# Performance work log

Measured on AMD Instinct MI355X. Metric: run time of the kernel, lower is better.

## Reference

```python
import jax, jax.numpy as jnp
import numpy as np

D, FIN1, CL1_F, CL1_K, CL2_F, CL2_K, FC1_F, FC2_F = 4096, 1, 32, 25, 64, 25, 512, 10
B = 64
NNZ1, NNZ2 = D * 8, (D // 2) * 8
LMAX = 2.0  # lmax_L of a normalized graph Laplacian
FC1FIN = CL2_F * (D // 4)


def setup_inputs() -> dict:
    key = jax.random.key(0)
    ks = jax.random.split(key, 16)
    def lin(kw, fout, fin):
        scale = np.sqrt(2.0 / (fin + fout)).astype(np.float32)
        return jax.random.uniform(kw, (fout, fin), jnp.float32, -scale, scale)
    V2 = D // 2
    return {
        "x": jax.random.normal(ks[0], (B, D, FIN1), jnp.float32),
        "L1_rows": jax.random.randint(ks[1], (NNZ1,), 0, D),
        "L1_cols": jax.random.randint(ks[2], (NNZ1,), 0, D),
        "L1_vals": jax.random.normal(ks[3], (NNZ1,), jnp.float32) * 0.1,
        "L2_rows": jax.random.randint(ks[4], (NNZ2,), 0, V2),
        "L2_cols": jax.random.randint(ks[5], (NNZ2,), 0, V2),
        "L2_vals": jax.random.normal(ks[6], (NNZ2,), jnp.float32) * 0.1,
        "cl1_W": lin(ks[7], CL1_F, CL1_K * FIN1),
        "cl1_b": jnp.zeros((CL1_F,), jnp.float32),
        "cl2_W": lin(ks[8], CL2_F, CL2_K * CL1_F),
        "cl2_b": jnp.zeros((CL2_F,), jnp.float32),
        "fc1_W": lin(ks[9], FC1_F, FC1FIN),
        "fc1_b": jnp.zeros((FC1_F,), jnp.float32),
        "fc2_W": lin(ks[10], FC2_F, FC1_F),
        "fc2_b": jnp.zeros((FC2_F,), jnp.float32),
    }


def _cheby_conv(x, rows, cols, vals, W, b, K):
    # x: [B, V, Fin]; sparse rescaled Laplacian Ls = (2/lmax)*L - I applied as SpMM.
    Bn, V, Fin = x.shape
    x0 = jnp.transpose(x, (1, 2, 0)).reshape(V, Fin * Bn)  # [V, Fin*B]
    coef = jnp.asarray(2.0 / LMAX, x.dtype)

    def Ls(z):  # (2/lmax) * L @ z - z, via segment-sum SpMM
        return coef * jax.ops.segment_sum(vals[:, None] * z[cols], rows, num_segments=V) - z

    xs = [x0]
    if K > 1:
        x1 = Ls(x0)
        xs.append(x1)
    for _ in range(2, K):
        x2 = 2.0 * Ls(x1) - x0
        xs.append(x2)
        x0, x1 = x1, x2
    xk = jnp.stack(xs, 0).reshape(K, V, Fin, Bn)        # [K, V, Fin, B]
    xk = jnp.transpose(xk, (3, 1, 2, 0)).reshape(Bn * V, Fin * K)
    y = xk @ W.T + b
    return y.reshape(Bn, V, -1)


def _max_pool(x, p):
    # max-pool over node dim with stride p (matches MaxPool1d over permuted layout)
    Bn, V, F = x.shape
    return x.reshape(Bn, V // p, p, F).max(axis=2)


def reference(x, L1_rows, L1_cols, L1_vals, L2_rows, L2_cols, L2_vals,
              cl1_W, cl1_b, cl2_W, cl2_b, fc1_W, fc1_b, fc2_W, fc2_b):
    h = _cheby_conv(x, L1_rows, L1_cols, L1_vals, cl1_W, cl1_b, CL1_K)
    h = jax.nn.relu(h)
    h = _max_pool(h, 2)
    h = _cheby_conv(h, L2_rows, L2_cols, L2_vals, cl2_W, cl2_b, CL2_K)
    h = jax.nn.relu(h)
    h = _max_pool(h, 2)
    h = h.reshape(-1, FC1FIN)
    h = jax.nn.relu(h @ fc1_W.T + fc1_b)
    # dropout d=0.0 (eval/deterministic) -> identity
    return h @ fc2_W.T + fc2_b
```

## Files before the change

kernel.cpp:

```cpp
#include <hip/hip_runtime.h>
#include <hip/hip_bf16.h>

#define V1 4096
#define V2 2048
#define NNZ1 32768
#define NNZ2 16384
#define WCAP 48

typedef unsigned short u16;
typedef unsigned int u32;
typedef __attribute__((ext_vector_type(8))) short bf16x8;
typedef __attribute__((ext_vector_type(4))) float f32x4;

static __device__ __forceinline__ float bf2f(u16 u) {
  union { u32 i; float f; } c; c.i = ((u32)u) << 16; return c.f;
}
static __device__ __forceinline__ u16 f2bf(float f) {
  union { u32 i; float f; } c; c.f = f;
  u32 r = c.i + 0x7FFFu + ((c.i >> 16) & 1u);
  return (u16)(r >> 16);
}

__global__ void k_hist(const int* __restrict__ L1r, const int* __restrict__ L2r,
                       const float* __restrict__ W2, u16* __restrict__ Wh,
                       u16* __restrict__ Wl,
                       int* __restrict__ cnt1, int* __restrict__ cnt2) {
  int lt = blockIdx.x, t = threadIdx.x;
  if (lt < 128) {
    atomicAdd(&cnt1[L1r[lt * 256 + t]], 1);
  } else if (lt < 192) {
    atomicAdd(&cnt2[L2r[(lt - 128) * 256 + t]], 1);
  } else {
    int idx = (lt - 192) * 256 + t;
    int f = idx / 800;
    int kap = idx - f * 800;
    int k = kap >> 5, fin = kap & 31;
    float w = W2[f * 800 + fin * 25 + k];
    u16 hi = f2bf(w);
    Wh[idx] = hi;
    Wl[idx] = f2bf(w - bf2f(hi));
  }
}

__global__ void k_scan(int* __restrict__ cnt1, int* __restrict__ rs1,
                       int* __restrict__ cnt2, int* __restrict__ rs2,
                       int* __restrict__ slotOf1, int* __restrict__ rowOf1,
                       int* __restrict__ slotOf2, int* __restrict__ rowOf2) {
  __shared__ int sums[256];
  __shared__ int degS[V1];
  __shared__ int hist[64];
  __shared__ int hb[64];
  int t = threadIdx.x;
  int* cnt; int* rs; int* slotOf; int* rowOf; int V, NT, nnz;
  if (blockIdx.x == 0) { cnt = cnt1; rs = rs1; slotOf = slotOf1; rowOf = rowOf1; V = V1; NT = 1024; nnz = NNZ1; }
  else                 { cnt = cnt2; rs = rs2; slotOf = slotOf2; rowOf = rowOf2; V = V2; NT = 512;  nnz = NNZ2; }
  int chunk = V / 256, base = t * chunk, s = 0;
  for (int i = 0; i < chunk; ++i) { int c = cnt[base + i]; degS[base + i] = c; s += c; }
  sums[t] = s;
  if (t < 64) hist[t] = 0;
  __syncthreads();
  if (t == 0) {
    int run = 0;
    for (int i = 0; i < 256; ++i) { int c = sums[i]; sums[i] = run; run += c; }
  }
  __syncthreads();
  int pfx = sums[t];
  for (int i = 0; i < chunk; ++i) {
    int c = degS[base + i];
    rs[base + i] = pfx;
    cnt[base + i] = pfx;
    pfx += c;
  }
  if (t == 0) rs[V] = nnz;
  for (int i = 0; i < chunk; ++i) {
    int d = degS[base + i]; if (d > 63) d = 63;
    atomicAdd(&hist[d], 1);
  }
  __syncthreads();
  if (t == 0) {
    int run = 0;
    for (int d = 63; d >= 0; --d) { hb[d] = run; run += hist[d]; }
  }
  __syncthreads();
  for (int i = 0; i < chunk; ++i) {
    int v = base + i;
    int d = degS[v]; if (d > 63) d = 63;
    int r = atomicAdd(&hb[d], 1);
    int slot = (r & 3) * NT + (r >> 2);
    slotOf[v] = slot;
    rowOf[slot] = v;
  }
}

__global__ void k_scatter(const int* __restrict__ L1r, const int* __restrict__ L1c,
                          const float* __restrict__ L1v,
                          const int* __restrict__ L2r, const int* __restrict__ L2c,
                          const float* __restrict__ L2v,
                          int* __restrict__ cur1, const int* __restrict__ rs1,
                          const int* __restrict__ slotOf1, float2* __restrict__ ell1,
                          int* __restrict__ cur2, const int* __restrict__ rs2,
                          const int* __restrict__ slotOf2, float2* __restrict__ ell2) {
  int lt = blockIdx.x, t = threadIdx.x;
  if (lt < 128) {
    int e = lt * 256 + t;
    int row = L1r[e];
    int pos = atomicAdd(&cur1[row], 1);
    int w = pos - rs1[row];
    if (w < WCAP)
      ell1[(size_t)w * V1 + slotOf1[row]] = make_float2(L1v[e], __int_as_float(L1c[e] * 4));
  } else {
    int e = (lt - 128) * 256 + t;
    int row = L2r[e];
    int pos = atomicAdd(&cur2[row], 1);
    int w = pos - rs2[row];
    if (w < WCAP)
      ell2[(size_t)w * V2 + slotOf2[row]] = make_float2(L2v[e], __int_as_float(L2c[e] * 16));
  }
}

__global__ void __launch_bounds__(1024) k_l1rec(
    const float* __restrict__ x, const int* __restrict__ rs1,
    const int* __restrict__ rowOf1, const float2* __restrict__ ell1,
    u16* __restrict__ T1) {
  __shared__ float fa[V1];
  const int b = blockIdx.x, t = threadIdx.x;
#pragma unroll
  for (int j = 0; j < 4; ++j) {
    int v = t + j * 1024;
    float xv = x[(size_t)b * V1 + v];
    fa[v] = xv;
    T1[((size_t)b) * V1 + v] = f2bf(xv);
  }
  int vj[4];
#pragma unroll
  for (int j = 0; j < 4; ++j) vj[j] = rowOf1[t + j * 1024];
  int bound = rs1[vj[0] + 1] - rs1[vj[0]];
  if (bound > WCAP) bound = WCAP;
  float t2r[4];
  __syncthreads();
  for (int k = 1; k < 25; ++k) {
    float acc[4] = {0.f, 0.f, 0.f, 0.f};
    for (int w = 0; w < bound; ++w) {
      const float2* ep = ell1 + (size_t)w * V1 + t;
#pragma unroll
      for (int j = 0; j < 4; ++j) {
        float2 ev = ep[j * 1024];
        int ub = __float_as_int(ev.y);
        float av = *(const float*)((const char*)fa + ub);
        acc[j] = fmaf(ev.x, av, acc[j]);
      }
    }
    __syncthreads();
#pragma unroll
    for (int j = 0; j < 4; ++j) {
      float old = fa[vj[j]];
      float z = acc[j] - old;
      if (k > 1) z = 2.f * z - t2r[j];
      t2r[j] = old;
      fa[vj[j]] = z;
    }
    __syncthreads();
#pragma unroll
    for (int j = 0; j < 4; ++j) {
      int v = t + j * 1024;
      T1[((size_t)k * 64 + b) * V1 + v] = f2bf(fa[v]);
    }
  }
}

__global__ void k_conv1(const u16* __restrict__ T1, const float* __restrict__ W1,
                        const float* __restrict__ b1, float* __restrict__ z0) {
  __shared__ float w1s[800];
  __shared__ float b1s[32];
  const int b = blockIdx.x & 63, uc = blockIdx.x >> 6, t = threadIdx.x;
  for (int idx = t; idx < 800; idx += 256) w1s[idx] = W1[idx];
  if (t < 32) b1s[t] = b1[t];
  __syncthreads();
  const int u = uc * 256 + t;
  float a1[25], a2[25];
#pragma unroll
  for (int k = 0; k < 25; ++k) {
    u32 w = *(const u32*)&T1[((size_t)k * 64 + b) * V1 + 2 * u];
    a1[k] = bf2f((u16)w);
    a2[k] = bf2f((u16)(w >> 16));
  }
  float mout[32];
#pragma unroll
  for (int f = 0; f < 32; ++f) {
    float s1 = b1s[f], s2 = b1s[f];
#pragma unroll
    for (int k = 0; k < 25; ++k) {
      float w = w1s[f * 25 + k];
      s1 = fmaf(a1[k], w, s1);
      s2 = fmaf(a2[k], w, s2);
    }
    mout[f] = fmaxf(fmaxf(s1, 0.f), fmaxf(s2, 0.f));
  }
  float4* dst = (float4*)&z0[((size_t)b * V2 + u) * 32];
#pragma unroll
  for (int q = 0; q < 8; ++q)
    dst[q] = make_float4(mout[4 * q], mout[4 * q + 1], mout[4 * q + 2], mout[4 * q + 3]);
}

__global__ void __launch_bounds__(512, 4) k_l2rec(
    const float* __restrict__ z0, const int* __restrict__ rs2,
    const int* __restrict__ rowOf2, const float2* __restrict__ ell2,
    u16* __restrict__ T2, int b0, int bs) {
  __shared__ float TkS[V2 * 4];
  const int bl = blockIdx.x % bs, fg = blockIdx.x / bs;
  const int b = b0 + bl, f0 = fg * 4;
  const int t = threadIdx.x;
  const size_t M = (size_t)bs * V2;
  const size_t mb = (size_t)bl * V2;
#pragma unroll
  for (int j = 0; j < 4; ++j) {
    int v = t + j * 512;
    float4 xv = *(const float4*)&z0[((size_t)b * V2 + v) * 32 + f0];
    *(float4*)&TkS[v * 4] = xv;
    u32 lo = (u32)f2bf(xv.x) | ((u32)f2bf(xv.y) << 16);
    u32 hi = (u32)f2bf(xv.z) | ((u32)f2bf(xv.w) << 16);
    *(uint2*)&T2[((size_t)fg * M + mb + v) * 4] = make_uint2(lo, hi);
  }
  int vj[4];
#pragma unroll
  for (int j = 0; j < 4; ++j) vj[j] = rowOf2[t + j * 512];
  int bound = rs2[vj[0] + 1] - rs2[vj[0]];
  if (bound > WCAP) bound = WCAP;
  float4 t2r[4];
  __syncthreads();
  for (int k = 1; k < 25; ++k) {
    float4 acc[4];
#pragma unroll
    for (int j = 0; j < 4; ++j) acc[j] = make_float4(0.f, 0.f, 0.f, 0.f);
    for (int w = 0; w < bound; ++w) {
      const float2* ep = ell2 + (size_t)w * V2 + t;
#pragma unroll
      for (int j = 0; j < 4; ++j) {
        float2 ev = ep[j * 512];
        int ub = __float_as_int(ev.y);
        float4 tv = *(const float4*)((const char*)TkS + ub);
        acc[j].x = fmaf(ev.x, tv.x, acc[j].x);
        acc[j].y = fmaf(ev.x, tv.y, acc[j].y);
        acc[j].z = fmaf(ev.x, tv.z, acc[j].z);
        acc[j].w = fmaf(ev.x, tv.w, acc[j].w);
      }
    }
    __syncthreads();
#pragma unroll
    for (int j = 0; j < 4; ++j) {
      float4 old = *(const float4*)&TkS[vj[j] * 4];
      float4 z;
      z.x = acc[j].x - old.x; z.y = acc[j].y - old.y;
      z.z = acc[j].z - old.z; z.w = acc[j].w - old.w;
      if (k > 1) {
        z.x = 2.f * z.x - t2r[j].x; z.y = 2.f * z.y - t2r[j].y;
        z.z = 2.f * z.z - t2r[j].z; z.w = 2.f * z.w - t2r[j].w;
      }
      t2r[j] = old;
      *(float4*)&TkS[vj[j] * 4] = z;
    }
    __syncthreads();
#pragma unroll
    for (int j = 0; j < 4; ++j) {
      int v = t + j * 512;
      float4 zz = *(const float4*)&TkS[v * 4];
      u32 lo = (u32)f2bf(zz.x) | ((u32)f2bf(zz.y) << 16);
      u32 hi = (u32)f2bf(zz.z) | ((u32)f2bf(zz.w) << 16);
      *(uint2*)&T2[(((size_t)k * 8 + fg) * M + mb + v) * 4] = make_uint2(lo, hi);
    }
  }
}

__global__ void __launch_bounds__(256) k_conv2mm(
    const u16* __restrict__ T2, const u16* __restrict__ Wh, const u16* __restrict__ Wl,
    const float* __restrict__ b2, u16* __restrict__ h2h, u16* __restrict__ h2l,
    int b0, int bs) {
  const int t = threadIdx.x;
  const int wid = t >> 6, lane = t & 63;
  const int ln = lane & 15, kg = lane >> 4;
  const size_t M = (size_t)bs * V2;
  const int mBlk = blockIdx.x * 128;
  const int bl = mBlk >> 11;
  const int v0 = mBlk & (V2 - 1);
  const int m0 = mBlk + wid * 32;
  const int vw = v0 + wid * 32;

  f32x4 acc[2][4];
#pragma unroll
  for (int nt = 0; nt < 4; ++nt) {
    float bv = b2[nt * 16 + ln];
    acc[0][nt] = (f32x4){bv, bv, bv, bv};
    acc[1][nt] = acc[0][nt];
  }

  for (int kc = 0; kc < 25; ++kc) {
    const int coff = kc * 32 + kg * 8;
    bf16x8 bh[4], blo[4];
#pragma unroll
    for (int nt = 0; nt < 4; ++nt) {
      bh[nt]  = *(const bf16x8*)(Wh + (size_t)(nt * 16 + ln) * 800 + coff);
      blo[nt] = *(const bf16x8*)(Wl + (size_t)(nt * 16 + ln) * 800 + coff);
    }
#pragma unroll
    for (int sp = 0; sp < 2; ++sp) {
      const u16* ap = T2 + ((size_t)(kc * 8 + kg * 2) * M + (size_t)(m0 + sp * 16 + ln)) * 4;
      uint2 alo = *(const uint2*)ap;
      uint2 ahi = *(const uint2*)(ap + M * 4);
      union { uint4 u; bf16x8 v; } ac;
      ac.u = make_uint4(alo.x, alo.y, ahi.x, ahi.y);
#pragma unroll
      for (int nt = 0; nt < 4; ++nt) {
        acc[sp][nt] = __builtin_amdgcn_mfma_f32_16x16x32_bf16(ac.v, bh[nt], acc[sp][nt], 0, 0, 0);
        acc[sp][nt] = __builtin_amdgcn_mfma_f32_16x16x32_bf16(ac.v, blo[nt], acc[sp][nt], 0, 0, 0);
      }
    }
  }
  const int b = b0 + bl;
  u16* hh = h2h + (size_t)b * 65536;
  u16* hl = h2l + (size_t)b * 65536;
#pragma unroll
  for (int sp = 0; sp < 2; ++sp) {
    int u = ((vw + sp * 16) >> 1) + kg * 2;
#pragma unroll
    for (int nt = 0; nt < 4; ++nt) {
      int f = nt * 16 + ln;
      float p0 = fmaxf(fmaxf(acc[sp][nt].x, acc[sp][nt].y), 0.f);
      float p1 = fmaxf(fmaxf(acc[sp][nt].z, acc[sp][nt].w), 0.f);
      u16 h0 = f2bf(p0), h1 = f2bf(p1);
      hh[(size_t)u * 64 + f] = h0;
      hh[(size_t)(u + 1) * 64 + f] = h1;
      hl[(size_t)u * 64 + f] = f2bf(p0 - bf2f(h0));
      hl[(size_t)(u + 1) * 64 + f] = f2bf(p1 - bf2f(h1));
    }
  }
}

__global__ void __launch_bounds__(256) k_fc1mm(
    const u16* __restrict__ h2h, const u16* __restrict__ h2l,
    const float* __restrict__ fW1, float* __restrict__ fc1o) {
  __shared__ u16 ahS[64 * 128];
  __shared__ u16 alS[64 * 128];
  const int t = threadIdx.x;
  const int wid = t >> 6, lane = t & 63;
  const int ln = lane & 15, kg = lane >> 4;
  const int jg = blockIdx.x & 7, ksp = blockIdx.x >> 3;
  const int j = (jg * 4 + wid) * 16 + ln;
  const int k0 = ksp * 2048;

  f32x4 acc[4];
#pragma unroll
  for (int bt = 0; bt < 4; ++bt) acc[bt] = (f32x4){0.f, 0.f, 0.f, 0.f};

  for (int sc = 0; sc < 16; ++sc) {
    const int kc = k0 + sc * 128;
    __syncthreads();
    for (int idx = t; idx < 1024; idx += 256) {
      int row = idx >> 4, unit = idx & 15;
      int lb = row * 256 + ((unit * 16) ^ ((row & 7) << 4));
      *(uint4*)((char*)ahS + lb) = *(const uint4*)(h2h + (size_t)row * 65536 + kc + unit * 8);
      *(uint4*)((char*)alS + lb) = *(const uint4*)(h2l + (size_t)row * 65536 + kc + unit * 8);
    }
    __syncthreads();
#pragma unroll
    for (int ks = 0; ks < 4; ++ks) {
      const float* wp = fW1 + (size_t)j * 65536 + kc + ks * 32 + kg * 8;
      float4 w0 = *(const float4*)wp;
      float4 w1 = *(const float4*)(wp + 4);
      float wa[8] = {w0.x, w0.y, w0.z, w0.w, w1.x, w1.y, w1.z, w1.w};
      bf16x8 bh, bl;
#pragma unroll
      for (int i = 0; i < 8; ++i) {
        u16 hi = f2bf(wa[i]);
        ((u16*)&bh)[i] = (short)hi;
        ((u16*)&bl)[i] = (short)f2bf(wa[i] - bf2f(hi));
      }
      const int kb = ks * 64 + kg * 16;
#pragma unroll
      for (int bt = 0; bt < 4; ++bt) {
        int row = bt * 16 + ln;
        int lb = row * 256 + (kb ^ ((row & 7) << 4));
        bf16x8 ah = *(const bf16x8*)((const char*)ahS + lb);
        bf16x8 al = *(const bf16x8*)((const char*)alS + lb);
        acc[bt] = __builtin_amdgcn_mfma_f32_16x16x32_bf16(ah, bh, acc[bt], 0, 0, 0);
        acc[bt] = __builtin_amdgcn_mfma_f32_16x16x32_bf16(ah, bl, acc[bt], 0, 0, 0);
        acc[bt] = __builtin_amdgcn_mfma_f32_16x16x32_bf16(al, bh, acc[bt], 0, 0, 0);
      }
    }
  }
#pragma unroll
  for (int bt = 0; bt < 4; ++bt) {
#pragma unroll
    for (int r = 0; r < 4; ++r) {
      atomicAdd(&fc1o[(size_t)j * 64 + bt * 16 + kg * 4 + r], acc[bt][r]);
    }
  }
}

__global__ void __launch_bounds__(256) k_fc2(
    const float* __restrict__ fc1o, const float* __restrict__ fb1,
    const float* __restrict__ fW2, const float* __restrict__ fb2,
    float* __restrict__ out) {
  __shared__ float red[256];
  const int c = blockIdx.x, t = threadIdx.x;
  const int b = t & 63, g = t >> 6;
  float s = 0.f;
  for (int j = g * 128; j < g * 128 + 128; ++j) {
    float a = fmaxf(fc1o[j * 64 + b] + fb1[j], 0.f);
    s = fmaf(a, fW2[c * 512 + j], s);
  }
  red[t] = s;
  __syncthreads();
  if (t < 64) {
    out[b * 10 + c] = red[t] + red[t + 64] + red[t + 128] + red[t + 192] + fb2[c];
  }
}

extern "C" void kernel_launch(void* const* d_in, const int* in_sizes, int n_in,
                              void* d_out, int out_size, void* d_ws, size_t ws_size,
                              hipStream_t stream) {
  const float* x    = (const float*)d_in[0];
  const int* L1r    = (const int*)d_in[1];
  const int* L1c    = (const int*)d_in[2];
  const float* L1v  = (const float*)d_in[3];
  const int* L2r    = (const int*)d_in[4];
  const int* L2c    = (const int*)d_in[5];
  const float* L2v  = (const float*)d_in[6];
  const float* W1   = (const float*)d_in[7];
  const float* b1   = (const float*)d_in[8];
  const float* W2   = (const float*)d_in[9];
  const float* b2   = (const float*)d_in[10];
  const float* fW1  = (const float*)d_in[11];
  const float* fb1  = (const float*)d_in[12];
  const float* fW2  = (const float*)d_in[13];
  const float* fb2  = (const float*)d_in[14];
  float* out = (float*)d_out;

  float* Wf = (float*)d_ws;
  size_t off = 0;
  auto alloc = [&](size_t n) { float* q = Wf + off; off += n; return q; };
  int* cnt1    = (int*)alloc(4096);
  int* rs1     = (int*)alloc(4104);
  int* cnt2    = (int*)alloc(2048);
  int* rs2     = (int*)alloc(2056);
  int* slotOf1 = (int*)alloc(4096);
  int* rowOf1  = (int*)alloc(4096);
  int* slotOf2 = (int*)alloc(2048);
  int* rowOf2  = (int*)alloc(2048);
  u16* Wh      = (u16*)alloc(25600);
  u16* Wl      = (u16*)alloc(25600);
  float* fc1o  = alloc(32768);
  float2* ell1 = (float2*)alloc((size_t)WCAP * V1 * 2);
  float2* ell2 = (float2*)alloc((size_t)WCAP * V2 * 2);
  float* z0    = alloc(4194304);
  u16* h2h     = (u16*)alloc(2097152);
  u16* h2l     = (u16*)alloc(2097152);
  size_t fixedB = off * 4;

  int ns = 8;
  for (int c = 1; c <= 8; c <<= 1) {
    size_t t2b = (size_t)V2 * (64 / c) * 800 * 2;
    size_t big = t2b > 16777216ull ? t2b : 16777216ull;
    if (fixedB + big + 65536 <= ws_size) { ns = c; break; }
  }
  const int bs = 64 / ns;
  u16* T1 = (u16*)(Wf + off);
  u16* T2 = (u16*)(Wf + off);

  hipMemsetAsync(cnt1, 0, 4096 * sizeof(int), stream);
  hipMemsetAsync(cnt2, 0, 2048 * sizeof(int), stream);
  hipMemsetAsync(fc1o, 0, 32768 * sizeof(float), stream);
  hipMemsetAsync(ell1, 0, (size_t)WCAP * V1 * 8, stream);
  hipMemsetAsync(ell2, 0, (size_t)WCAP * V2 * 8, stream);

  k_hist<<<392, 256, 0, stream>>>(L1r, L2r, W2, Wh, Wl, cnt1, cnt2);
  k_scan<<<2, 256, 0, stream>>>(cnt1, rs1, cnt2, rs2, slotOf1, rowOf1, slotOf2, rowOf2);
  k_scatter<<<192, 256, 0, stream>>>(L1r, L1c, L1v, L2r, L2c, L2v,
                                     cnt1, rs1, slotOf1, ell1,
                                     cnt2, rs2, slotOf2, ell2);

  k_l1rec<<<64, 1024, 0, stream>>>(x, rs1, rowOf1, ell1, T1);
  k_conv1<<<512, 256, 0, stream>>>(T1, W1, b1, z0);

  for (int s = 0; s < ns; ++s) {
    int b0 = s * bs;
    k_l2rec<<<bs * 8, 512, 0, stream>>>(z0, rs2, rowOf2, ell2, T2, b0, bs);
    k_conv2mm<<<bs * 16, 256, 0, stream>>>(T2, Wh, Wl, b2, h2h, h2l, b0, bs);
  }

  k_fc1mm<<<256, 256, 0, stream>>>(h2h, h2l, fW1, fc1o);
  k_fc2<<<10, 256, 0, stream>>>(fc1o, fb1, fW2, fb2, out);
}
```

Measured before the change: 729.9 us.

## Reorder layer-2 ELL entries by column group and replace fc1 atomics with split reduction

Adds a per-row pass that sorts each layer-2 ELL row's entries by a column-derived group and rotates them per slot. The likely aim is to reduce LDS bank conflicts or contention when k_l2rec gathers neighbours. Separately, fc1's split-K partial sums are now written to a 32-way partial buffer and summed by a new reduction kernel instead of using global float atomics. The cost is two extra small kernels, an extra memset and more workspace, which may shift the T2 staging-slice choice.

```diff
diff --git a/kernel.cpp b/kernel.cpp
--- a/kernel.cpp
+++ b/kernel.cpp
@@ -118,6 +118,31 @@
   }
 }
 
+__global__ void k_reorder(const int* __restrict__ rs2, const int* __restrict__ rowOf2,
+                          const float2* __restrict__ ell2, float2* __restrict__ ellT) {
+  int s = blockIdx.x * 256 + threadIdx.x;
+  int v = rowOf2[s];
+  int d = rs2[v + 1] - rs2[v];
+  if (d > WCAP) d = WCAP;
+  if (d <= 0) return;
+  int cnt[8] = {0, 0, 0, 0, 0, 0, 0, 0};
+  for (int w = 0; w < d; ++w) {
+    float2 e = ell2[w * V2 + s];
+    int g = (__float_as_int(e.y) >> 4) & 7;
+    cnt[g]++;
+  }
+  int pfx[8]; int run = 0;
+  for (int g = 0; g < 8; ++g) { pfx[g] = run; run += cnt[g]; }
+  int rot = (s & 7) % d;
+  for (int w = 0; w < d; ++w) {
+    float2 e = ell2[w * V2 + s];
+    int g = (__float_as_int(e.y) >> 4) & 7;
+    int pos = pfx[g]++;
+    int wp = pos + rot; if (wp >= d) wp -= d;
+    ellT[wp * V2 + s] = e;
+  }
+}
+
 __global__ void __launch_bounds__(1024) k_l1rec(
     const float* __restrict__ x, const int* __restrict__ rs1,
     const int* __restrict__ rowOf1, const float2* __restrict__ ell1,
@@ -337,7 +362,7 @@
 
 __global__ void __launch_bounds__(256) k_fc1mm(
     const u16* __restrict__ h2h, const u16* __restrict__ h2l,
-    const float* __restrict__ fW1, float* __restrict__ fc1o) {
+    const float* __restrict__ fW1, float* __restrict__ P) {
   __shared__ u16 ahS[64 * 128];
   __shared__ u16 alS[64 * 128];
   const int t = threadIdx.x;
@@ -391,9 +416,16 @@
   for (int bt = 0; bt < 4; ++bt) {
 #pragma unroll
     for (int r = 0; r < 4; ++r) {
-      atomicAdd(&fc1o[(size_t)j * 64 + bt * 16 + kg * 4 + r], acc[bt][r]);
-    }
-  }
+      P[(size_t)ksp * 32768 + (size_t)j * 64 + bt * 16 + kg * 4 + r] = acc[bt][r];
+    }
+  }
+}
+
+__global__ void k_red(const float* __restrict__ P, float* __restrict__ fc1o) {
+  int idx = blockIdx.x * 256 + threadIdx.x;
+  float s = 0.f;
+  for (int k = 0; k < 32; ++k) s += P[(size_t)k * 32768 + idx];
+  fc1o[idx] = s;
 }
 
 __global__ void __launch_bounds__(256) k_fc2(
@@ -451,6 +483,8 @@
   float* fc1o  = alloc(32768);
   float2* ell1 = (float2*)alloc((size_t)WCAP * V1 * 2);
   float2* ell2 = (float2*)alloc((size_t)WCAP * V2 * 2);
+  float2* ellT = (float2*)alloc((size_t)WCAP * V2 * 2);
+  float* P     = alloc(32 * 32768);
   float* z0    = alloc(4194304);
   u16* h2h     = (u16*)alloc(2097152);
   u16* h2l     = (u16*)alloc(2097152);
@@ -468,25 +502,27 @@
 
   hipMemsetAsync(cnt1, 0, 4096 * sizeof(int), stream);
   hipMemsetAsync(cnt2, 0, 2048 * sizeof(int), stream);
-  hipMemsetAsync(fc1o, 0, 32768 * sizeof(float), stream);
   hipMemsetAsync(ell1, 0, (size_t)WCAP * V1 * 8, stream);
   hipMemsetAsync(ell2, 0, (size_t)WCAP * V2 * 8, stream);
+  hipMemsetAsync(ellT, 0, (size_t)WCAP * V2 * 8, stream);
 
   k_hist<<<392, 256, 0, stream>>>(L1r, L2r, W2, Wh, Wl, cnt1, cnt2);
   k_scan<<<2, 256, 0, stream>>>(cnt1, rs1, cnt2, rs2, slotOf1, rowOf1, slotOf2, rowOf2);
   k_scatter<<<192, 256, 0, stream>>>(L1r, L1c, L1v, L2r, L2c, L2v,
                                      cnt1, rs1, slotOf1, ell1,
                                      cnt2, rs2, slotOf2, ell2);
+  k_reorder<<<8, 256, 0, stream>>>(rs2, rowOf2, ell2, ellT);
 
   k_l1rec<<<64, 1024, 0, stream>>>(x, rs1, rowOf1, ell1, T1);
   k_conv1<<<512, 256, 0, stream>>>(T1, W1, b1, z0);
 
   for (int s = 0; s < ns; ++s) {
     int b0 = s * bs;
-    k_l2rec<<<bs * 8, 512, 0, stream>>>(z0, rs2, rowOf2, ell2, T2, b0, bs);
+    k_l2rec<<<bs * 8, 512, 0, stream>>>(z0, rs2, rowOf2, ellT, T2, b0, bs);
     k_conv2mm<<<bs * 16, 256, 0, stream>>>(T2, Wh, Wl, b2, h2h, h2l, b0, bs);
   }
 
-  k_fc1mm<<<256, 256, 0, stream>>>(h2h, h2l, fW1, fc1o);
+  k_fc1mm<<<256, 256, 0, stream>>>(h2h, h2l, fW1, P);
+  k_red<<<128, 256, 0, stream>>>(P, fc1o);
   k_fc2<<<10, 256, 0, stream>>>(fc1o, fb1, fW2, fb2, out);
 }
```

New measurement: 742.0 us. No clear change (+1.7%).
